# Kernel tuning notes

Measured on AMD Instinct MI355X. Metric: run time of the kernel, lower is better.

## Reference

```python
import jax, jax.numpy as jnp
import numpy as np

B, N, M, F, K = 32, 256, 64, 128, 64
N_INTERACT_RES, N_ATOM_RES = 3, 2


def ssp(x):
    # shifted softplus, PhysNet activation
    return jax.nn.softplus(x) - jnp.log(2.0).astype(x.dtype)


def res_block(h, W1, b1, W2, b2):
    # PhysNet residual layer: h + W2 @ ssp(W1 @ ssp(h) + b1) + b2
    t = ssp(h)
    t = ssp(t @ W1.T + b1)
    return h + t @ W2.T + b2


def setup_inputs() -> dict:
    key = jax.random.key(0)
    ks = jax.random.split(key, 20)
    sF = 1.0 / np.sqrt(F)
    sK = 1.0 / np.sqrt(K)
    return {
        "x": jax.random.normal(ks[0], (B, N, F), jnp.float32),
        "rbf": jax.random.uniform(ks[1], (B, N, M, K), jnp.float32),
        "neighbor": jax.random.randint(ks[2], (B, N, M), 0, N, jnp.int32),
        "k2f_W": jax.random.normal(ks[3], (F, K), jnp.float32) * sK,  # no bias
        "Wi": jax.random.normal(ks[4], (F, F), jnp.float32) * sF,
        "bi": jnp.zeros((F,), jnp.float32),
        "ires_W1": jax.random.normal(ks[5], (N_INTERACT_RES, F, F), jnp.float32) * sF,
        "ires_b1": jnp.zeros((N_INTERACT_RES, F), jnp.float32),
        "ires_W2": jax.random.normal(ks[6], (N_INTERACT_RES, F, F), jnp.float32) * sF,
        "ires_b2": jnp.zeros((N_INTERACT_RES, F), jnp.float32),
        "Wint": jax.random.normal(ks[7], (F, F), jnp.float32) * sF,
        "bint": jnp.zeros((F,), jnp.float32),
        "u_gate": jnp.ones((F,), jnp.float32),
        "ares_W1": jax.random.normal(ks[8], (N_ATOM_RES, F, F), jnp.float32) * sF,
        "ares_b1": jnp.zeros((N_ATOM_RES, F), jnp.float32),
        "ares_W2": jax.random.normal(ks[9], (N_ATOM_RES, F, F), jnp.float32) * sF,
        "ares_b2": jnp.zeros((N_ATOM_RES, F), jnp.float32),
    }


def reference(x, rbf, neighbor, k2f_W, Wi, bi, ires_W1, ires_b1, ires_W2, ires_b2,
              Wint, bint, u_gate, ares_W1, ares_b1, ares_W2, ares_b2):
    b, n, f = x.shape
    m = neighbor.shape[2]
    xa = ssp(x)                                            # (B,N,F)
    g = jnp.einsum('bnmk,fk->bnmf', rbf, k2f_W)            # RBF filter (B,N,M,F)
    xi = ssp(xa @ Wi.T + bi)                               # self message
    # gather neighbor features: xj[b,n,m,:] = xa[b, neighbor[b,n,m], :]
    idx = jnp.broadcast_to(neighbor.reshape(b, n * m)[:, :, None], (b, n * m, f))
    xj = jnp.take_along_axis(xa, idx, axis=1).reshape(b, n, m, f)
    xj = jnp.sum(xj * g, axis=2)                           # aggregate over neighbors
    v = xi + xj
    for l in range(ires_W1.shape[0]):
        v = res_block(v, ires_W1[l], ires_b1[l], ires_W2[l], ires_b2[l])
    v = ssp(v)
    out = u_gate * x + (v @ Wint.T + bint)
    for l in range(ares_W1.shape[0]):
        out = res_block(out, ares_W1[l], ares_b1[l], ares_W2[l], ares_b2[l])
    return out
```

## Files before the change

kernel.cpp:

```cpp
#include <hip/hip_runtime.h>
#include <math.h>

#define PB 32
#define PN 256
#define PM 64
#define PF 128
#define PK 64
#define ROWS (PB*PN)
#define NTOT (ROWS*PF)

#define OFF_K2F  0
#define OFF_WI   8192
#define OFF_IW1  24576
#define OFF_IW2  73728
#define OFF_WINT 122880
#define OFF_AW1  139264
#define OFF_AW2  172032
#define TOTAL_W  204800

#define XPITCH 136

typedef __attribute__((ext_vector_type(4))) float  floatx4;
typedef __attribute__((ext_vector_type(8))) short  shortx8;

__device__ __forceinline__ unsigned short f2b(float f){
    union { float f; unsigned int i; } c; c.f = f;
    unsigned int x = c.i;
    return (unsigned short)((x + 0x7fffu + ((x >> 16) & 1u)) >> 16);
}
__device__ __forceinline__ float bf2f(unsigned short u){
    union { unsigned int i; float f; } c; c.i = ((unsigned int)u) << 16; return c.f;
}
__device__ __forceinline__ float sspf(float x){
    return fmaxf(x, 0.0f) + log1pf(expf(-fabsf(x))) - 0.69314718055994531f;
}
__device__ __forceinline__ shortx8 pack8(float4 a, float4 b){
    shortx8 r;
    r[0]=(short)f2b(a.x); r[1]=(short)f2b(a.y); r[2]=(short)f2b(a.z); r[3]=(short)f2b(a.w);
    r[4]=(short)f2b(b.x); r[5]=(short)f2b(b.y); r[6]=(short)f2b(b.z); r[7]=(short)f2b(b.w);
    return r;
}

__global__ __launch_bounds__(256) void k_pre(const float* __restrict__ x,
                                             const float* __restrict__ k2f,
                                             const float* __restrict__ Wi,
                                             const float* __restrict__ iW1,
                                             const float* __restrict__ iW2,
                                             const float* __restrict__ Wint,
                                             const float* __restrict__ aW1,
                                             const float* __restrict__ aW2,
                                             float* __restrict__ xa_f,
                                             unsigned short* __restrict__ xa_b,
                                             unsigned short* __restrict__ Wb){
    int i = blockIdx.x * 256 + threadIdx.x;
    if (i < NTOT){
        float v = sspf(x[i]);
        xa_f[i] = v;
        xa_b[i] = f2b(v);
        return;
    }
    int j = i - NTOT;
    if (j >= TOTAL_W) return;
    float v;
    if      (j < OFF_WI)   v = k2f[j - OFF_K2F];
    else if (j < OFF_IW1)  v = Wi[j - OFF_WI];
    else if (j < OFF_IW2)  v = iW1[j - OFF_IW1];
    else if (j < OFF_WINT) v = iW2[j - OFF_IW2];
    else if (j < OFF_AW1)  v = Wint[j - OFF_WINT];
    else if (j < OFF_AW2)  v = aW1[j - OFF_AW1];
    else                   v = aW2[j - OFF_AW2];
    Wb[j] = f2b(v);
}

__global__ __launch_bounds__(256) void k_msg(const float* __restrict__ rbf,
                                             const int* __restrict__ nbr,
                                             const unsigned short* __restrict__ Wk2f,
                                             const float* __restrict__ xa_f,
                                             float* __restrict__ xj){
    const int tid  = threadIdx.x;
    const int t    = tid >> 6;
    const int bid  = blockIdx.x;
    const int b    = bid >> 8;
    const int lane = tid & 63;
    const int quad = lane >> 4;
    const int l16  = lane & 15;

    __shared__ float red[4][PF];

    const float* rrow = rbf + (size_t)bid * (PM*PK) + (size_t)(t*16 + l16) * PK;
    float4 r0 = *(const float4*)(rrow + quad*8);
    float4 r1 = *(const float4*)(rrow + quad*8 + 4);
    float4 r2 = *(const float4*)(rrow + 32 + quad*8);
    float4 r3 = *(const float4*)(rrow + 32 + quad*8 + 4);
    int4 nb = *(const int4*)(nbr + (size_t)bid*PM + t*16 + quad*4);

    const float* xab = xa_f + (size_t)b * PN * PF;

    shortx8 afrag0 = pack8(r0, r1);
    shortx8 afrag1 = pack8(r2, r3);

    float s[8];
    #pragma unroll
    for (int ft = 0; ft < 8; ++ft){
        const unsigned short* wrow = Wk2f + (size_t)(ft*16 + l16) * PK;
        shortx8 b0 = *(const shortx8*)(wrow +  0 + quad*8);
        shortx8 b1 = *(const shortx8*)(wrow + 32 + quad*8);
        floatx4 acc = {0.f, 0.f, 0.f, 0.f};
        acc = __builtin_amdgcn_mfma_f32_16x16x32_bf16(afrag0, b0, acc, 0, 0, 0);
        acc = __builtin_amdgcn_mfma_f32_16x16x32_bf16(afrag1, b1, acc, 0, 0, 0);
        const int col = ft*16 + l16;
        float v =  acc[0] * xab[(size_t)nb.x*PF + col];
        v       += acc[1] * xab[(size_t)nb.y*PF + col];
        v       += acc[2] * xab[(size_t)nb.z*PF + col];
        v       += acc[3] * xab[(size_t)nb.w*PF + col];
        s[ft] = v;
    }

    #pragma unroll
    for (int ft = 0; ft < 8; ++ft){
        float v = s[ft];
        v += __shfl_xor(v, 16, 64);
        v += __shfl_xor(v, 32, 64);
        if (quad == 0) red[t][ft*16 + l16] = v;
    }
    __syncthreads();
    if (tid < PF){
        xj[(size_t)bid*PF + tid] = red[0][tid] + red[1][tid] + red[2][tid] + red[3][tid];
    }
}

__device__ __forceinline__ void gemm2(const unsigned short* __restrict__ W,
                                      int l16, int quad, int ftbase,
                                      const shortx8 a[4], floatx4 acc[2]){
    #pragma unroll
    for (int f = 0; f < 2; ++f){
        const unsigned short* wrow = W + (size_t)((ftbase+f)*16 + l16) * PF;
        floatx4 c = {0.f, 0.f, 0.f, 0.f};
        #pragma unroll
        for (int ks = 0; ks < 4; ++ks){
            shortx8 bf = *(const shortx8*)(wrow + ks*32 + quad*8);
            c = __builtin_amdgcn_mfma_f32_16x16x32_bf16(a[ks], bf, c, 0, 0, 0);
        }
        acc[f] = c;
    }
}

__device__ __forceinline__ void relayout(unsigned short* Tls,
                                         const unsigned short t16[8],
                                         int l16, int quad, int ftbase,
                                         shortx8 a[4]){
    #pragma unroll
    for (int f = 0; f < 2; ++f)
        #pragma unroll
        for (int r = 0; r < 4; ++r)
            Tls[(quad*4 + r)*XPITCH + (ftbase+f)*16 + l16] = t16[f*4 + r];
    __syncthreads();
    #pragma unroll
    for (int ks = 0; ks < 4; ++ks)
        a[ks] = *(const shortx8*)(Tls + l16*XPITCH + ks*32 + quad*8);
}

__global__ __launch_bounds__(256) void k_chain(const unsigned short* __restrict__ xa_b,
                                               const float* __restrict__ xj,
                                               const float* __restrict__ x,
                                               const unsigned short* __restrict__ Wb,
                                               const float* __restrict__ bi,
                                               const float* __restrict__ ib1,
                                               const float* __restrict__ ib2,
                                               const float* __restrict__ bint,
                                               const float* __restrict__ ugate,
                                               const float* __restrict__ ab1,
                                               const float* __restrict__ ab2,
                                               float* __restrict__ out){
    const int tid  = threadIdx.x;
    const int wave = tid >> 6;
    const int lane = tid & 63;
    const int quad = lane >> 4;
    const int l16  = lane & 15;
    const int ftb  = wave*2;
    const int row0 = blockIdx.x * 16;

    __shared__ unsigned short Tls[2][16 * XPITCH];
    int p = 0;

    int col[2];
    #pragma unroll
    for (int f = 0; f < 2; ++f) col[f] = (ftb+f)*16 + l16;

    const unsigned short* inrow = xa_b + (size_t)(row0 + l16) * PF;
    shortx8 a[4];
    #pragma unroll
    for (int ks = 0; ks < 4; ++ks)
        a[ks] = *(const shortx8*)(inrow + ks*32 + quad*8);

    floatx4 acc[2];
    float V[8];
    unsigned short t16[8];

    gemm2(Wb + OFF_WI, l16, quad, ftb, a, acc);
    #pragma unroll
    for (int f = 0; f < 2; ++f)
        #pragma unroll
        for (int r = 0; r < 4; ++r){
            size_t idx = (size_t)(row0 + quad*4 + r)*PF + col[f];
            float of = sspf(acc[f][r] + bi[col[f]]) + xj[idx];
            V[f*4+r] = of;
            t16[f*4+r] = f2b(sspf(of));
        }
    relayout(Tls[p], t16, l16, quad, ftb, a); p ^= 1;

    for (int l = 0; l < 3; ++l){
        gemm2(Wb + OFF_IW1 + l*PF*PF, l16, quad, ftb, a, acc);
        #pragma unroll
        for (int f = 0; f < 2; ++f)
            #pragma unroll
            for (int r = 0; r < 4; ++r)
                t16[f*4+r] = f2b(sspf(acc[f][r] + ib1[l*PF + col[f]]));
        relayout(Tls[p], t16, l16, quad, ftb, a); p ^= 1;

        gemm2(Wb + OFF_IW2 + l*PF*PF, l16, quad, ftb, a, acc);
        #pragma unroll
        for (int f = 0; f < 2; ++f)
            #pragma unroll
            for (int r = 0; r < 4; ++r){
                V[f*4+r] += acc[f][r] + ib2[l*PF + col[f]];
                t16[f*4+r] = f2b(sspf(V[f*4+r]));
            }
        relayout(Tls[p], t16, l16, quad, ftb, a); p ^= 1;
    }

    gemm2(Wb + OFF_WINT, l16, quad, ftb, a, acc);
    #pragma unroll
    for (int f = 0; f < 2; ++f)
        #pragma unroll
        for (int r = 0; r < 4; ++r){
            size_t idx = (size_t)(row0 + quad*4 + r)*PF + col[f];
            float o = ugate[col[f]] * x[idx] + acc[f][r] + bint[col[f]];
            V[f*4+r] = o;
            t16[f*4+r] = f2b(sspf(o));
        }
    relayout(Tls[p], t16, l16, quad, ftb, a); p ^= 1;

    #pragma unroll
    for (int l = 0; l < 2; ++l){
        gemm2(Wb + OFF_AW1 + l*PF*PF, l16, quad, ftb, a, acc);
        #pragma unroll
        for (int f = 0; f < 2; ++f)
            #pragma unroll
            for (int r = 0; r < 4; ++r)
                t16[f*4+r] = f2b(sspf(acc[f][r] + ab1[l*PF + col[f]]));
        relayout(Tls[p], t16, l16, quad, ftb, a); p ^= 1;

        gemm2(Wb + OFF_AW2 + l*PF*PF, l16, quad, ftb, a, acc);
        if (l == 0){
            #pragma unroll
            for (int f = 0; f < 2; ++f)
                #pragma unroll
                for (int r = 0; r < 4; ++r){
                    V[f*4+r] += acc[f][r] + ab2[l*PF + col[f]];
                    t16[f*4+r] = f2b(sspf(V[f*4+r]));
                }
            relayout(Tls[p], t16, l16, quad, ftb, a); p ^= 1;
        } else {
            #pragma unroll
            for (int f = 0; f < 2; ++f)
                #pragma unroll
                for (int r = 0; r < 4; ++r){
                    size_t idx = (size_t)(row0 + quad*4 + r)*PF + col[f];
                    out[idx] = V[f*4+r] + acc[f][r] + ab2[l*PF + col[f]];
                }
        }
    }
}

extern "C" void kernel_launch(void* const* d_in, const int* in_sizes, int n_in,
                              void* d_out, int out_size, void* d_ws, size_t ws_size,
                              hipStream_t stream){
    const float* x     = (const float*)d_in[0];
    const float* rbf   = (const float*)d_in[1];
    const int*   nbr   = (const int*)d_in[2];
    const float* k2fW  = (const float*)d_in[3];
    const float* Wi    = (const float*)d_in[4];
    const float* bi    = (const float*)d_in[5];
    const float* iW1   = (const float*)d_in[6];
    const float* ib1   = (const float*)d_in[7];
    const float* iW2   = (const float*)d_in[8];
    const float* ib2   = (const float*)d_in[9];
    const float* Wint  = (const float*)d_in[10];
    const float* bint  = (const float*)d_in[11];
    const float* ugate = (const float*)d_in[12];
    const float* aW1   = (const float*)d_in[13];
    const float* ab1   = (const float*)d_in[14];
    const float* aW2   = (const float*)d_in[15];
    const float* ab2   = (const float*)d_in[16];

    char* ws = (char*)d_ws;
    unsigned short* xa_b = (unsigned short*)ws;
    float*          xa_f = (float*)(ws + (2ull  << 20));
    float*          xj   = (float*)(ws + (6ull  << 20));
    unsigned short* Wb   = (unsigned short*)(ws + (10ull << 20));

    k_pre<<<(NTOT + TOTAL_W + 255)/256, 256, 0, stream>>>(
        x, k2fW, Wi, iW1, iW2, Wint, aW1, aW2, xa_f, xa_b, Wb);
    k_msg<<<ROWS, 256, 0, stream>>>(rbf, nbr, Wb + OFF_K2F, xa_f, xj);
    k_chain<<<ROWS/16, 256, 0, stream>>>(xa_b, xj, x, Wb,
                                         bi, ib1, ib2, bint, ugate, ab1, ab2,
                                         (float*)d_out);
}
```

Baseline: 322.5 us.

## Stage per-batch xa in LDS and process 32 atoms per k_msg block

Each k_msg block now handles 32 atoms of one batch with 512 threads. It copies the whole 128 KB fp32 xa slab for that batch into shared memory so the neighbor gathers read LDS instead of global memory. The bf16 k2f weight fragments are held in registers across atoms, and the next atom's rbf and neighbor indices are prefetched while the current one computes. The price is heavy LDS use (one block per CU at most), only 256 blocks in the grid, and a block-wide barrier on every atom iteration.

After: 288.1 us. 10.7% less time.

```diff
diff --git a/kernel.cpp b/kernel.cpp
--- a/kernel.cpp
+++ b/kernel.cpp
@@ -19,6 +19,8 @@
 #define TOTAL_W  204800
 
 #define XPITCH 136
+
+#define APB 32
 
 typedef __attribute__((ext_vector_type(4))) float  floatx4;
 typedef __attribute__((ext_vector_type(8))) short  shortx8;
@@ -72,60 +74,113 @@
     Wb[j] = f2b(v);
 }
 
-__global__ __launch_bounds__(256) void k_msg(const float* __restrict__ rbf,
+__global__ __launch_bounds__(512) void k_msg(const float* __restrict__ rbf,
                                              const int* __restrict__ nbr,
                                              const unsigned short* __restrict__ Wk2f,
                                              const float* __restrict__ xa_f,
                                              float* __restrict__ xj){
     const int tid  = threadIdx.x;
-    const int t    = tid >> 6;
-    const int bid  = blockIdx.x;
-    const int b    = bid >> 8;
+    const int w    = tid >> 6;
     const int lane = tid & 63;
     const int quad = lane >> 4;
     const int l16  = lane & 15;
-
-    __shared__ float red[4][PF];
-
-    const float* rrow = rbf + (size_t)bid * (PM*PK) + (size_t)(t*16 + l16) * PK;
-    float4 r0 = *(const float4*)(rrow + quad*8);
-    float4 r1 = *(const float4*)(rrow + quad*8 + 4);
-    float4 r2 = *(const float4*)(rrow + 32 + quad*8);
-    float4 r3 = *(const float4*)(rrow + 32 + quad*8 + 4);
-    int4 nb = *(const int4*)(nbr + (size_t)bid*PM + t*16 + quad*4);
-
-    const float* xab = xa_f + (size_t)b * PN * PF;
-
-    shortx8 afrag0 = pack8(r0, r1);
-    shortx8 afrag1 = pack8(r2, r3);
-
-    float s[8];
+    const int slot = w >> 2;
+    const int t    = w & 3;
+
+    const int blk   = blockIdx.x;
+    const int b     = blk >> 3;
+    const int n0    = (blk & 7) * APB;
+    const int atom0 = b * PN + n0;
+
+    __shared__ float xa_s[PN * PF];
+    __shared__ float red[2][2][4][PF];
+
+    const int rowoff = (t*16 + l16) * PK + quad*8;
+    {
+    }
+    const float* rb0 = rbf + (size_t)(atom0 + slot) * (PM*PK) + rowoff;
+    float4 r0 = *(const float4*)(rb0);
+    float4 r1 = *(const float4*)(rb0 + 4);
+    float4 r2 = *(const float4*)(rb0 + 32);
+    float4 r3 = *(const float4*)(rb0 + 36);
+    int4  nb  = *(const int4*)(nbr + (size_t)(atom0 + slot)*PM + t*16 + quad*4);
+
+    const float* src = xa_f + (size_t)b * (PN*PF);
+    #pragma unroll
+    for (int p = 0; p < 16; ++p){
+        int idx = p*2048 + tid*4;
+        *(float4*)(&xa_s[idx]) = *(const float4*)(src + idx);
+    }
+
+    shortx8 bf0[8], bf1[8];
     #pragma unroll
     for (int ft = 0; ft < 8; ++ft){
         const unsigned short* wrow = Wk2f + (size_t)(ft*16 + l16) * PK;
-        shortx8 b0 = *(const shortx8*)(wrow +  0 + quad*8);
-        shortx8 b1 = *(const shortx8*)(wrow + 32 + quad*8);
-        floatx4 acc = {0.f, 0.f, 0.f, 0.f};
-        acc = __builtin_amdgcn_mfma_f32_16x16x32_bf16(afrag0, b0, acc, 0, 0, 0);
-        acc = __builtin_amdgcn_mfma_f32_16x16x32_bf16(afrag1, b1, acc, 0, 0, 0);
-        const int col = ft*16 + l16;
-        float v =  acc[0] * xab[(size_t)nb.x*PF + col];
-        v       += acc[1] * xab[(size_t)nb.y*PF + col];
-        v       += acc[2] * xab[(size_t)nb.z*PF + col];
-        v       += acc[3] * xab[(size_t)nb.w*PF + col];
-        s[ft] = v;
-    }
-
-    #pragma unroll
-    for (int ft = 0; ft < 8; ++ft){
-        float v = s[ft];
-        v += __shfl_xor(v, 16, 64);
-        v += __shfl_xor(v, 32, 64);
-        if (quad == 0) red[t][ft*16 + l16] = v;
-    }
+        bf0[ft] = *(const shortx8*)(wrow + quad*8);
+        bf1[ft] = *(const shortx8*)(wrow + 32 + quad*8);
+    }
+
     __syncthreads();
-    if (tid < PF){
-        xj[(size_t)bid*PF + tid] = red[0][tid] + red[1][tid] + red[2][tid] + red[3][tid];
+
+    for (int it = 0; it < APB/2; ++it){
+        const int a = slot + it*2;
+
+        shortx8 af0 = pack8(r0, r1);
+        shortx8 af1 = pack8(r2, r3);
+        const int j0 = nb.x, j1 = nb.y, j2 = nb.z, j3 = nb.w;
+
+        if (it + 1 < APB/2){
+            const float* rbn = rbf + (size_t)(atom0 + a + 2) * (PM*PK) + rowoff;
+            r0 = *(const float4*)(rbn);
+            r1 = *(const float4*)(rbn + 4);
+            r2 = *(const float4*)(rbn + 32);
+            r3 = *(const float4*)(rbn + 36);
+            nb = *(const int4*)(nbr + (size_t)(atom0 + a + 2)*PM + t*16 + quad*4);
+        }
+
+        floatx4 acc8[8];
+        #pragma unroll
+        for (int ft = 0; ft < 8; ++ft){
+            floatx4 c = {0.f, 0.f, 0.f, 0.f};
+            c = __builtin_amdgcn_mfma_f32_16x16x32_bf16(af0, bf0[ft], c, 0, 0, 0);
+            c = __builtin_amdgcn_mfma_f32_16x16x32_bf16(af1, bf1[ft], c, 0, 0, 0);
+            acc8[ft] = c;
+        }
+
+        const float* rp0 = xa_s + (size_t)j0*PF + l16;
+        const float* rp1 = xa_s + (size_t)j1*PF + l16;
+        const float* rp2 = xa_s + (size_t)j2*PF + l16;
+        const float* rp3 = xa_s + (size_t)j3*PF + l16;
+        float s[8];
+        #pragma unroll
+        for (int ft = 0; ft < 8; ++ft){
+            float v =  acc8[ft][0] * rp0[ft*16];
+            v       += acc8[ft][1] * rp1[ft*16];
+            v       += acc8[ft][2] * rp2[ft*16];
+            v       += acc8[ft][3] * rp3[ft*16];
+            s[ft] = v;
+        }
+
+        #pragma unroll
+        for (int ft = 0; ft < 8; ++ft){
+            float v = s[ft];
+            v += __shfl_xor(v, 16, 64);
+            v += __shfl_xor(v, 32, 64);
+            if (quad == 0) red[it & 1][slot][t][ft*16 + l16] = v;
+        }
+        __syncthreads();
+
+        if (t == 0){
+            const float* rd = &red[it & 1][slot][0][0];
+            float2 v0 = *(const float2*)(rd + 0*PF + 2*lane);
+            float2 v1 = *(const float2*)(rd + 1*PF + 2*lane);
+            float2 v2 = *(const float2*)(rd + 2*PF + 2*lane);
+            float2 v3 = *(const float2*)(rd + 3*PF + 2*lane);
+            float2 o;
+            o.x = v0.x + v1.x + v2.x + v3.x;
+            o.y = v0.y + v1.y + v2.y + v3.y;
+            *(float2*)(xj + (size_t)(atom0 + a)*PF + 2*lane) = o;
+        }
     }
 }
 
@@ -302,7 +357,7 @@
 
     k_pre<<<(NTOT + TOTAL_W + 255)/256, 256, 0, stream>>>(
         x, k2fW, Wi, iW1, iW2, Wint, aW1, aW2, xa_f, xa_b, Wb);
-    k_msg<<<ROWS, 256, 0, stream>>>(rbf, nbr, Wb + OFF_K2F, xa_f, xj);
+    k_msg<<<PB * (PN/APB), 512, 0, stream>>>(rbf, nbr, Wb + OFF_K2F, xa_f, xj);
     k_chain<<<ROWS/16, 256, 0, stream>>>(xa_b, xj, x, Wb,
                                          bi, ib1, ib2, bint, ugate, ab1, ab2,
                                          (float*)d_out);
```
